# Optimization experiments

Hardware: AMD Instinct MI355X
Metric: run time of the kernel (lower is better)

Reference implementation:

```python
import jax, jax.numpy as jnp
import numpy as np

PATTERN_BOOST = 1.2


def setup_inputs() -> dict:
    key = jax.random.key(0)
    k1, k2 = jax.random.split(key)
    B, S, L = 64, 8192, 24
    logits = jax.random.normal(k1, (B, S, L), dtype=jnp.float32)
    labels = jax.random.randint(k2, (B, S, L), 0, 2).astype(jnp.int32)  # binary multi-label targets
    attention_mask = jnp.ones((B, S), dtype=jnp.float32)
    return {"logits": logits, "labels": labels, "attention_mask": attention_mask}


def reference(logits, labels, attention_mask):
    y = labels.astype(logits.dtype)
    # numerically-stable BCE-with-logits, elementwise (reduction='none')
    loss = jnp.maximum(logits, 0) - logits * y + jnp.log1p(jnp.exp(-jnp.abs(logits)))
    # vectorized pattern boost: positions i in [0, S-2] where step i and i+1 both have any punct
    has_punct = labels.sum(axis=-1) > 0                      # [B, S]
    pair = has_punct[:, :-1] & has_punct[:, 1:]              # [B, S-1]
    boost = 1.0 + pair.astype(logits.dtype) * (PATTERN_BOOST - 1.0)
    boost = jnp.pad(boost, ((0, 0), (0, 1)), constant_values=1.0)  # last timestep never boosted
    loss = loss * boost[:, :, None]
    mask = attention_mask[:, :, None].astype(logits.dtype)   # [B, S, 1]
    return (loss * mask).sum() / mask.sum()
```

## Files before the change

kernel.cpp:

```cpp
#include <hip/hip_runtime.h>

constexpr int Bdim = 64;
constexpr int S = 8192;
constexpr int L = 24;
constexpr int NPOS = Bdim * S;
constexpr int NCHUNK = NPOS * (L / 4);
constexpr float BOOST = 1.2f;
constexpr int NBLK_B = 256;

__device__ __forceinline__ float bce(float x, float yi) {
    return fmaxf(x, 0.0f) - x * yi + log1pf(expf(-fabsf(x)));
}

__global__ __launch_bounds__(256) void pal_bce(
    const float* __restrict__ logits,
    const int*   __restrict__ labels,
    float*         __restrict__ loss_ws,
    unsigned char* __restrict__ hp_ws)
{
    __shared__ float psum[768];
    __shared__ float plab[768];
    const int t = threadIdx.x;
    const size_t base = (size_t)blockIdx.x * 768;

#pragma unroll
    for (int k = 0; k < 3; ++k) {
        const size_t c = base + (size_t)t + 256 * k;
        float4 lg = ((const float4*)logits)[c];
        int4   lb = ((const int4*)labels)[c];
        float s = 0.0f;
        s += bce(lg.x, (float)lb.x);
        s += bce(lg.y, (float)lb.y);
        s += bce(lg.z, (float)lb.z);
        s += bce(lg.w, (float)lb.w);
        psum[t + 256 * k] = s;
        plab[t + 256 * k] = (float)(lb.x + lb.y + lb.z + lb.w);
    }
    __syncthreads();

    if (t < 128) {
        float ls = 0.0f, lab = 0.0f;
#pragma unroll
        for (int j = 0; j < 6; ++j) {
            ls  += psum[6 * t + j];
            lab += plab[6 * t + j];
        }
        const size_t p = (size_t)blockIdx.x * 128 + t;
        loss_ws[p] = ls;
        hp_ws[p]   = (lab > 0.0f) ? 1 : 0;
    }
}

__global__ __launch_bounds__(256) void pal_boost(
    const float*         __restrict__ loss_ws,
    const unsigned char* __restrict__ hp_ws,
    const float*         __restrict__ mask,
    double*              __restrict__ partials)
{
    double lsum = 0.0, msum = 0.0;
    const int stride = gridDim.x * blockDim.x;
    for (int p = blockIdx.x * blockDim.x + threadIdx.x; p < NPOS; p += stride) {
        const int s = p & (S - 1);
        float ls = loss_ws[p];
        float m  = mask[p];
        float boost = (s < S - 1 && hp_ws[p] && hp_ws[p + 1]) ? BOOST : 1.0f;
        lsum += (double)(ls * boost * m);
        msum += (double)m;
    }
    __shared__ double sl[256], sm[256];
    sl[threadIdx.x] = lsum;
    sm[threadIdx.x] = msum;
    __syncthreads();
    for (int off = 128; off > 0; off >>= 1) {
        if (threadIdx.x < off) {
            sl[threadIdx.x] += sl[threadIdx.x + off];
            sm[threadIdx.x] += sm[threadIdx.x + off];
        }
        __syncthreads();
    }
    if (threadIdx.x == 0) {
        partials[2 * blockIdx.x]     = sl[0];
        partials[2 * blockIdx.x + 1] = sm[0];
    }
}

__global__ __launch_bounds__(256) void pal_final(
    const double* __restrict__ partials,
    float*        __restrict__ out)
{
    const int t = threadIdx.x;
    double l = partials[2 * t];
    double m = partials[2 * t + 1];
    __shared__ double sl[256], sm[256];
    sl[t] = l; sm[t] = m;
    __syncthreads();
    for (int off = 128; off > 0; off >>= 1) {
        if (t < off) { sl[t] += sl[t + off]; sm[t] += sm[t + off]; }
        __syncthreads();
    }
    if (t == 0) out[0] = (float)(sl[0] / sm[0]);
}

extern "C" void kernel_launch(void* const* d_in, const int* in_sizes, int n_in,
                              void* d_out, int out_size, void* d_ws, size_t ws_size,
                              hipStream_t stream) {
    const float* logits = (const float*)d_in[0];
    const int*   labels = (const int*)d_in[1];
    const float* mask   = (const float*)d_in[2];
    float* out = (float*)d_out;

    char* ws = (char*)d_ws;
    float*         loss_ws  = (float*)ws;
    unsigned char* hp_ws    = (unsigned char*)(ws + (size_t)NPOS * sizeof(float));
    double*        partials = (double*)(ws + (size_t)NPOS * sizeof(float) + NPOS);

    pal_bce  <<<NPOS / 128, 256, 0, stream>>>(logits, labels, loss_ws, hp_ws);
    pal_boost<<<NBLK_B,     256, 0, stream>>>(loss_ws, hp_ws, mask, partials);
    pal_final<<<1,          256, 0, stream>>>(partials, out);
}
```

Before: 139.1 us.

## Fuse BCE and pattern-boost passes into one kernel with fast exp/log

Merges the per-position BCE kernel and the boost/mask reduction kernel into a single kernel. Each block computes the neighbour has-punct flag from shared memory, with thread 0 peeking at the next block's labels, and reduces with wave shuffles. This removes the intermediate loss/flag workspace round-trip and one launch. It also switches expf/log1pf to __expf/__logf, trading some accuracy for cheaper transcendentals. The final reduction now loops over thousands of per-block partials.

```diff
diff --git a/kernel.cpp b/kernel.cpp
--- a/kernel.cpp
+++ b/kernel.cpp
@@ -4,28 +4,46 @@
 constexpr int S = 8192;
 constexpr int L = 24;
 constexpr int NPOS = Bdim * S;
-constexpr int NCHUNK = NPOS * (L / 4);
+constexpr int POS_PER_BLK = 128;
+constexpr int NBLK = NPOS / POS_PER_BLK;
+constexpr int BLK_PER_ROW = S / POS_PER_BLK;
 constexpr float BOOST = 1.2f;
-constexpr int NBLK_B = 256;
 
-__device__ __forceinline__ float bce(float x, float yi) {
-    return fmaxf(x, 0.0f) - x * yi + log1pf(expf(-fabsf(x)));
+__device__ __forceinline__ float bce(float x, float y) {
+    float e = __expf(-fabsf(x));
+    float l = __logf(1.0f + e);
+    return fmaxf(x, 0.0f) - x * y + l;
 }
 
-__global__ __launch_bounds__(256) void pal_bce(
+__global__ __launch_bounds__(256) void pal_main(
     const float* __restrict__ logits,
     const int*   __restrict__ labels,
-    float*         __restrict__ loss_ws,
-    unsigned char* __restrict__ hp_ws)
+    const float* __restrict__ mask,
+    double*      __restrict__ partials)
 {
     __shared__ float psum[768];
     __shared__ float plab[768];
+    __shared__ unsigned char hp_next_sh;
+    __shared__ float wl[4], wm[4];
+
     const int t = threadIdx.x;
-    const size_t base = (size_t)blockIdx.x * 768;
+    const size_t cbase = (size_t)blockIdx.x * 768;
+
+    if (t == 0) {
+        int hn = 0;
+        if ((blockIdx.x & (BLK_PER_ROW - 1)) != BLK_PER_ROW - 1) {
+            const int4* nb = (const int4*)labels + cbase + 768;
+            int sn = 0;
+#pragma unroll
+            for (int j = 0; j < 6; ++j) { int4 v = nb[j]; sn += v.x + v.y + v.z + v.w; }
+            hn = (sn > 0) ? 1 : 0;
+        }
+        hp_next_sh = (unsigned char)hn;
+    }
 
 #pragma unroll
     for (int k = 0; k < 3; ++k) {
-        const size_t c = base + (size_t)t + 256 * k;
+        const size_t c = cbase + (size_t)t + 256 * k;
         float4 lg = ((const float4*)logits)[c];
         int4   lb = ((const int4*)labels)[c];
         float s = 0.0f;
@@ -38,49 +56,38 @@
     }
     __syncthreads();
 
-    if (t < 128) {
+    float contrib = 0.0f, m = 0.0f;
+    if (t < POS_PER_BLK) {
         float ls = 0.0f, lab = 0.0f;
 #pragma unroll
-        for (int j = 0; j < 6; ++j) {
-            ls  += psum[6 * t + j];
-            lab += plab[6 * t + j];
+        for (int j = 0; j < 6; ++j) { ls += psum[6 * t + j]; lab += plab[6 * t + j]; }
+        int hp = (lab > 0.0f);
+        int hpn;
+        if (t < POS_PER_BLK - 1) {
+            float ln = 0.0f;
+#pragma unroll
+            for (int j = 0; j < 6; ++j) ln += plab[6 * t + 6 + j];
+            hpn = (ln > 0.0f);
+        } else {
+            hpn = hp_next_sh;
         }
-        const size_t p = (size_t)blockIdx.x * 128 + t;
-        loss_ws[p] = ls;
-        hp_ws[p]   = (lab > 0.0f) ? 1 : 0;
+        float boost = (hp && hpn) ? BOOST : 1.0f;
+        m = mask[(size_t)blockIdx.x * POS_PER_BLK + t];
+        contrib = ls * boost * m;
     }
-}
 
-__global__ __launch_bounds__(256) void pal_boost(
-    const float*         __restrict__ loss_ws,
-    const unsigned char* __restrict__ hp_ws,
-    const float*         __restrict__ mask,
-    double*              __restrict__ partials)
-{
-    double lsum = 0.0, msum = 0.0;
-    const int stride = gridDim.x * blockDim.x;
-    for (int p = blockIdx.x * blockDim.x + threadIdx.x; p < NPOS; p += stride) {
-        const int s = p & (S - 1);
-        float ls = loss_ws[p];
-        float m  = mask[p];
-        float boost = (s < S - 1 && hp_ws[p] && hp_ws[p + 1]) ? BOOST : 1.0f;
-        lsum += (double)(ls * boost * m);
-        msum += (double)m;
+#pragma unroll
+    for (int off = 32; off > 0; off >>= 1) {
+        contrib += __shfl_down(contrib, off, 64);
+        m       += __shfl_down(m, off, 64);
     }
-    __shared__ double sl[256], sm[256];
-    sl[threadIdx.x] = lsum;
-    sm[threadIdx.x] = msum;
+    if ((t & 63) == 0) { wl[t >> 6] = contrib; wm[t >> 6] = m; }
     __syncthreads();
-    for (int off = 128; off > 0; off >>= 1) {
-        if (threadIdx.x < off) {
-            sl[threadIdx.x] += sl[threadIdx.x + off];
-            sm[threadIdx.x] += sm[threadIdx.x + off];
-        }
-        __syncthreads();
-    }
-    if (threadIdx.x == 0) {
-        partials[2 * blockIdx.x]     = sl[0];
-        partials[2 * blockIdx.x + 1] = sm[0];
+    if (t == 0) {
+        double Ls = (double)wl[0] + (double)wl[1] + (double)wl[2] + (double)wl[3];
+        double Ms = (double)wm[0] + (double)wm[1] + (double)wm[2] + (double)wm[3];
+        partials[2 * blockIdx.x]     = Ls;
+        partials[2 * blockIdx.x + 1] = Ms;
     }
 }
 
@@ -89,8 +96,11 @@
     float*        __restrict__ out)
 {
     const int t = threadIdx.x;
-    double l = partials[2 * t];
-    double m = partials[2 * t + 1];
+    double l = 0.0, m = 0.0;
+    for (int i = t; i < NBLK; i += 256) {
+        l += partials[2 * i];
+        m += partials[2 * i + 1];
+    }
     __shared__ double sl[256], sm[256];
     sl[t] = l; sm[t] = m;
     __syncthreads();
@@ -107,14 +117,9 @@
     const float* logits = (const float*)d_in[0];
     const int*   labels = (const int*)d_in[1];
     const float* mask   = (const float*)d_in[2];
-    float* out = (float*)d_out;
+    float*  out = (float*)d_out;
+    double* partials = (double*)d_ws;
 
-    char* ws = (char*)d_ws;
-    float*         loss_ws  = (float*)ws;
-    unsigned char* hp_ws    = (unsigned char*)(ws + (size_t)NPOS * sizeof(float));
-    double*        partials = (double*)(ws + (size_t)NPOS * sizeof(float) + NPOS);
-
-    pal_bce  <<<NPOS / 128, 256, 0, stream>>>(logits, labels, loss_ws, hp_ws);
-    pal_boost<<<NBLK_B,     256, 0, stream>>>(loss_ws, hp_ws, mask, partials);
-    pal_final<<<1,          256, 0, stream>>>(partials, out);
+    pal_main <<<NBLK, 256, 0, stream>>>(logits, labels, mask, partials);
+    pal_final<<<1,    256, 0, stream>>>(partials, out);
 }
```

After: 122.4 us. -12.0%, faster.
